# Performance work log

Measured on AMD Instinct MI355X. Metric: run time of the kernel, lower is better.

The kernel has to match this reference:

```python
import jax, jax.numpy as jnp
import numpy as np

B = 1024        # number of dialogs
MX_LEN = 110    # max utterances per dialog (alpha width hardcoded to 110 in source)
G_DIM = 512     # node feature dim
WP, WF = 10, 10 # past / future window
ALPHA_W = 110
NEG = -1e9


def setup_inputs() -> dict:
    key = jax.random.key(0)
    k1, k2, k3 = jax.random.split(key, 3)
    node_features = jax.random.normal(k1, (B, MX_LEN, G_DIM), dtype=jnp.float32)
    var = 2.0 / (G_DIM + G_DIM)  # matches torch init: normal_(0, var)
    weight = jax.random.normal(k2, (G_DIM, G_DIM), dtype=jnp.float32) * var
    text_len = jax.random.randint(k3, (B,), 1, MX_LEN + 1)
    return {"node_features": node_features, "weight": weight, "text_len": text_len}


def reference(node_features, weight, text_len):
    Bsz, L, D = node_features.shape
    # att_matrix[b, l] = weight @ node_features[b, l]
    att = jnp.einsum('de,ble->bld', weight, node_features)            # [B, L, D]
    # score[b, j, l] = att[b, l] . node_features[b, j]
    scores = jnp.einsum('bld,bjd->bjl', att, node_features)           # [B, J, Lkey]
    j = jnp.arange(L)[:, None]   # query position
    l = jnp.arange(L)[None, :]   # key position
    lens = text_len[:, None, None]                                    # [B, 1, 1]
    # window: s = max(0, j-wp), e = min(j+wf, cur_len-1); valid only for j < cur_len
    mask = (l >= j - WP) & (l <= j + WF) & (l <= lens - 1) & (j <= lens - 1)
    probs = jax.nn.softmax(jnp.where(mask, scores, NEG), axis=-1)
    probs = jnp.where(mask, probs, 0.0)                               # [B, L, L]
    # alpha is [mx_len, 110] per batch, zero outside window; stack over batch
    alpha = jnp.zeros((Bsz, L, ALPHA_W), dtype=probs.dtype).at[:, :, :L].set(probs)
    return alpha
```

## Files before the change

### kernel.cpp

```cpp
#include <hip/hip_runtime.h>
#include <stdint.h>

#define L_SZ 110
#define D_SZ 512
#define OUT_W 110
#define A_STRIDE 520
#define C_STRIDE 136
#define A_ROWS 112
#define ATT_ROWS 112
#define NF_ROWS 112
#define G3_ST 40

typedef __attribute__((ext_vector_type(8))) __bf16 bf16x8;
typedef __attribute__((ext_vector_type(4))) __bf16 bf16x4;
typedef __attribute__((ext_vector_type(4))) float f32x4;

__global__ __launch_bounds__(256) void wconv_kernel(const float* __restrict__ W,
                                                    __bf16* __restrict__ wbf) {
    int idx = blockIdx.x * 256 + threadIdx.x;
    float4 w = ((const float4*)W)[idx];
    bf16x4 o;
    o[0] = (__bf16)w.x; o[1] = (__bf16)w.y; o[2] = (__bf16)w.z; o[3] = (__bf16)w.w;
    ((bf16x4*)wbf)[idx] = o;
}

__global__ __launch_bounds__(256, 3) void att_gemm5_kernel(
    const float* __restrict__ nf, const __bf16* __restrict__ wbf,
    const int* __restrict__ tlenp, __bf16* __restrict__ attws,
    __bf16* __restrict__ nfbf)
{
    __shared__ __bf16 A_lds[112 * G3_ST];
    __shared__ __bf16 B_lds[128 * G3_ST];

    const int b   = blockIdx.y;
    const int cg  = blockIdx.x;
    const int tid = threadIdx.x;
    const int lane = tid & 63;
    const int wave = tid >> 6;
    const int l15  = lane & 15;
    const int quad = lane >> 4;

    int len = tlenp[b];
    if (len > L_SZ) len = L_SZ;
    if (len < 1) len = 1;
    const int T = (len + 15) >> 4;
    const int rows_needed = T << 4;

    const float* nfb = nf + (size_t)b * (L_SZ * D_SZ);

    const int r0 = tid >> 2;
    const int c8 = (tid & 3) << 3;
    const int rows2[2] = { r0, r0 + 64 };
    int stat[2];
    #pragma unroll
    for (int s = 0; s < 2; ++s) {
        int r = rows2[s];
        stat[s] = (r >= rows_needed) ? 0 : ((r < L_SZ) ? 1 : 2);
    }

    f32x4 acc[7][2];
    const f32x4 fz = {0.f, 0.f, 0.f, 0.f};
    #pragma unroll
    for (int m = 0; m < 7; ++m) { acc[m][0] = fz; acc[m][1] = fz; }

    float4 abuf[2][2];
    bf16x8 bbuf[2];

    auto load_tiles = [&](int k0) {
        #pragma unroll
        for (int s = 0; s < 2; ++s) {
            if (stat[s] == 1) {
                const float* ap = nfb + (size_t)rows2[s] * D_SZ + k0 + c8;
                abuf[s][0] = *(const float4*)ap;
                abuf[s][1] = *(const float4*)(ap + 4);
            }
            bbuf[s] = *(const bf16x8*)&wbf[(size_t)(cg * 128 + rows2[s]) * D_SZ + k0 + c8];
        }
    };
    auto store_tiles = [&](int kcur) {
        #pragma unroll
        for (int s = 0; s < 2; ++s) {
            if (stat[s]) {
                bf16x8 o;
                if (stat[s] == 1) {
                    o[0]=(__bf16)abuf[s][0].x; o[1]=(__bf16)abuf[s][0].y;
                    o[2]=(__bf16)abuf[s][0].z; o[3]=(__bf16)abuf[s][0].w;
                    o[4]=(__bf16)abuf[s][1].x; o[5]=(__bf16)abuf[s][1].y;
                    o[6]=(__bf16)abuf[s][1].z; o[7]=(__bf16)abuf[s][1].w;
                } else {
                    o[0]=o[1]=o[2]=o[3]=o[4]=o[5]=o[6]=o[7]=(__bf16)0.0f;
                }
                *(bf16x8*)&A_lds[rows2[s] * G3_ST + c8] = o;
                if (cg == 0) {
                    *(bf16x8*)&nfbf[((size_t)b * NF_ROWS + rows2[s]) * D_SZ + kcur + c8] = o;
                }
            }
            *(bf16x8*)&B_lds[rows2[s] * G3_ST + c8] = bbuf[s];
        }
    };

    load_tiles(0);
    for (int kt = 0; kt < 16; ++kt) {
        store_tiles(kt << 5);
        __syncthreads();
        if (kt < 15) load_tiles((kt + 1) << 5);
        bf16x8 bfr[2];
        #pragma unroll
        for (int ni = 0; ni < 2; ++ni)
            bfr[ni] = *(const bf16x8*)&B_lds[(wave * 32 + ni * 16 + l15) * G3_ST + quad * 8];
        #pragma unroll
        for (int m = 0; m < 7; ++m) {
            if (m < T) {
                bf16x8 af = *(const bf16x8*)&A_lds[(m * 16 + l15) * G3_ST + quad * 8];
                acc[m][0] = __builtin_amdgcn_mfma_f32_16x16x32_bf16(af, bfr[0], acc[m][0], 0, 0, 0);
                acc[m][1] = __builtin_amdgcn_mfma_f32_16x16x32_bf16(af, bfr[1], acc[m][1], 0, 0, 0);
            }
        }
        __syncthreads();
    }

    __bf16* tw = &A_lds[wave * 16 * G3_ST];
    const size_t obase = (size_t)b * (ATT_ROWS * D_SZ) + cg * 128 + wave * 32;
    const int erow = lane >> 2;
    const int ec8  = (lane & 3) << 3;
    #pragma unroll
    for (int m = 0; m < 7; ++m) {
        if (m < T) {
            #pragma unroll
            for (int ni = 0; ni < 2; ++ni)
                #pragma unroll
                for (int r = 0; r < 4; ++r)
                    tw[(quad * 4 + r) * G3_ST + ni * 16 + l15] = (__bf16)acc[m][ni][r];
            bf16x8 v = *(const bf16x8*)&tw[erow * G3_ST + ec8];
            *(bf16x8*)&attws[obase + (size_t)(m * 16 + erow) * D_SZ + ec8] = v;
        }
    }
}

__global__ __launch_bounds__(256) void band3_kernel(
    const __bf16* __restrict__ nfbf, const __bf16* __restrict__ attws,
    const int* __restrict__ tlenp, float* __restrict__ out)
{
    const int half = blockIdx.x;
    const int b = blockIdx.y;
    const int tid = threadIdx.x;
    const int lane = tid & 63;
    const int wave = tid >> 6;
    const int l15 = lane & 15;
    const int quad = lane >> 4;

    int len = tlenp[b];
    if (len > L_SZ) len = L_SZ;
    if (len < 1) len = 1;
    const int T = (len + 15) >> 4;

    const int tj = half * 4 + wave;
    if (tj >= T) return;

    float* outb = out + (size_t)b * (L_SZ * OUT_W);

    int jr = (tj << 4) + l15;
    if (jr > L_SZ - 1) jr = L_SZ - 1;
    const __bf16* apt = &nfbf[((size_t)b * NF_ROWS + jr) * D_SZ + (quad << 3)];

    bool tv[3];
    const __bf16* bpt[3];
    #pragma unroll
    for (int t = 0; t < 3; ++t) {
        int tl = tj - 1 + t;
        tv[t] = (tl >= 0) && (tl < T);
        bpt[t] = tv[t] ? &attws[((size_t)b * ATT_ROWS + (tl << 4) + l15) * D_SZ + (quad << 3)]
                       : apt;
    }

    const f32x4 fz = {0.f, 0.f, 0.f, 0.f};
    f32x4 accS[3] = {fz, fz, fz};

    bf16x8 afA, afB, bfA[3], bfB[3];
    afA = *(const bf16x8*)(apt);
    #pragma unroll
    for (int t = 0; t < 3; ++t) if (tv[t]) bfA[t] = *(const bf16x8*)(bpt[t]);

    #pragma unroll
    for (int kt = 0; kt < 16; ++kt) {
        const int knext = (kt + 1) << 5;
        if ((kt & 1) == 0) {
            if (kt < 15) {
                afB = *(const bf16x8*)(apt + knext);
                #pragma unroll
                for (int t = 0; t < 3; ++t) if (tv[t]) bfB[t] = *(const bf16x8*)(bpt[t] + knext);
            }
            #pragma unroll
            for (int t = 0; t < 3; ++t)
                if (tv[t]) accS[t] = __builtin_amdgcn_mfma_f32_16x16x32_bf16(afA, bfA[t], accS[t], 0, 0, 0);
        } else {
            if (kt < 15) {
                afA = *(const bf16x8*)(apt + knext);
                #pragma unroll
                for (int t = 0; t < 3; ++t) if (tv[t]) bfA[t] = *(const bf16x8*)(bpt[t] + knext);
            }
            #pragma unroll
            for (int t = 0; t < 3; ++t)
                if (tv[t]) accS[t] = __builtin_amdgcn_mfma_f32_16x16x32_bf16(afB, bfB[t], accS[t], 0, 0, 0);
        }
    }

    #pragma unroll
    for (int r = 0; r < 4; ++r) {
        int j = tj * 16 + quad * 4 + r;
        float v[3]; bool mk[3];
        float vmax = -3.0e38f;
        #pragma unroll
        for (int t = 0; t < 3; ++t) {
            int tl = tj - 1 + t;
            int l = tl * 16 + l15;
            bool in = tv[t] && (j < len) && (l < len)
                      && (l >= j - 10) && (l <= j + 10);
            float val = in ? accS[t][r] : -3.0e38f;
            mk[t] = in; v[t] = val;
            vmax = fmaxf(vmax, val);
        }
        #pragma unroll
        for (int s = 1; s < 16; s <<= 1)
            vmax = fmaxf(vmax, __shfl_xor(vmax, s, 16));
        float e[3]; float esum = 0.f;
        #pragma unroll
        for (int t = 0; t < 3; ++t) {
            e[t] = mk[t] ? __expf(v[t] - vmax) : 0.f;
            esum += e[t];
        }
        #pragma unroll
        for (int s = 1; s < 16; s <<= 1)
            esum += __shfl_xor(esum, s, 16);
        float inv = (esum > 0.f) ? (1.0f / esum) : 0.f;
        if (j < OUT_W) {
            #pragma unroll
            for (int t = 0; t < 3; ++t) {
                if (tv[t]) {
                    int l = (tj - 1 + t) * 16 + l15;
                    if (l < OUT_W) outb[(size_t)j * OUT_W + l] = e[t] * inv;
                }
            }
        }
    }
}

__global__ __launch_bounds__(256, 3) void att_gemm3_kernel(
    const float* __restrict__ nf, const __bf16* __restrict__ wbf,
    const int* __restrict__ tlenp, __bf16* __restrict__ attws)
{
    __shared__ __bf16 A_lds[112 * G3_ST];
    __shared__ __bf16 B_lds[128 * G3_ST];

    const int b   = blockIdx.y;
    const int cg  = blockIdx.x;
    const int tid = threadIdx.x;
    const int lane = tid & 63;
    const int wave = tid >> 6;
    const int l15  = lane & 15;
    const int quad = lane >> 4;

    int len = tlenp[b];
    if (len > L_SZ) len = L_SZ;
    if (len < 1) len = 1;
    const int T = (len + 15) >> 4;
    const int rows_needed = T << 4;

    const float* nfb = nf + (size_t)b * (L_SZ * D_SZ);

    const int r0 = tid >> 2;
    const int c8 = (tid & 3) << 3;
    const int rows2[2] = { r0, r0 + 64 };
    int stat[2];
    #pragma unroll
    for (int s = 0; s < 2; ++s) {
        int r = rows2[s];
        stat[s] = (r >= rows_needed) ? 0 : ((r < L_SZ) ? 1 : 2);
    }

    f32x4 acc[7][2];
    const f32x4 fz = {0.f, 0.f, 0.f, 0.f};
    #pragma unroll
    for (int m = 0; m < 7; ++m) { acc[m][0] = fz; acc[m][1] = fz; }

    float4 abuf[2][2];
    bf16x8 bbuf[2];

    auto load_tiles = [&](int k0) {
        #pragma unroll
        for (int s = 0; s < 2; ++s) {
            if (stat[s] == 1) {
                const float* ap = nfb + (size_t)rows2[s] * D_SZ + k0 + c8;
                abuf[s][0] = *(const float4*)ap;
                abuf[s][1] = *(const float4*)(ap + 4);
            }
            bbuf[s] = *(const bf16x8*)&wbf[(size_t)(cg * 128 + rows2[s]) * D_SZ + k0 + c8];
        }
    };
    auto store_tiles = [&]() {
        #pragma unroll
        for (int s = 0; s < 2; ++s) {
            if (stat[s]) {
                bf16x8 o;
                if (stat[s] == 1) {
                    o[0]=(__bf16)abuf[s][0].x; o[1]=(__bf16)abuf[s][0].y;
                    o[2]=(__bf16)abuf[s][0].z; o[3]=(__bf16)abuf[s][0].w;
                    o[4]=(__bf16)abuf[s][1].x; o[5]=(__bf16)abuf[s][1].y;
                    o[6]=(__bf16)abuf[s][1].z; o[7]=(__bf16)abuf[s][1].w;
                } else {
                    o[0]=o[1]=o[2]=o[3]=o[4]=o[5]=o[6]=o[7]=(__bf16)0.0f;
                }
                *(bf16x8*)&A_lds[rows2[s] * G3_ST + c8] = o;
            }
            *(bf16x8*)&B_lds[rows2[s] * G3_ST + c8] = bbuf[s];
        }
    };

    load_tiles(0);
    for (int kt = 0; kt < 16; ++kt) {
        store_tiles();
        __syncthreads();
        if (kt < 15) load_tiles((kt + 1) << 5);
        bf16x8 bfr[2];
        #pragma unroll
        for (int ni = 0; ni < 2; ++ni)
            bfr[ni] = *(const bf16x8*)&B_lds[(wave * 32 + ni * 16 + l15) * G3_ST + quad * 8];
        #pragma unroll
        for (int m = 0; m < 7; ++m) {
            if (m < T) {
                bf16x8 af = *(const bf16x8*)&A_lds[(m * 16 + l15) * G3_ST + quad * 8];
                acc[m][0] = __builtin_amdgcn_mfma_f32_16x16x32_bf16(af, bfr[0], acc[m][0], 0, 0, 0);
                acc[m][1] = __builtin_amdgcn_mfma_f32_16x16x32_bf16(af, bfr[1], acc[m][1], 0, 0, 0);
            }
        }
        __syncthreads();
    }

    __bf16* tw = &A_lds[wave * 16 * G3_ST];
    const size_t obase = (size_t)b * (ATT_ROWS * D_SZ) + cg * 128 + wave * 32;
    const int erow = lane >> 2;
    const int ec8  = (lane & 3) << 3;
    #pragma unroll
    for (int m = 0; m < 7; ++m) {
        if (m < T) {
            #pragma unroll
            for (int ni = 0; ni < 2; ++ni)
                #pragma unroll
                for (int r = 0; r < 4; ++r)
                    tw[(quad * 4 + r) * G3_ST + ni * 16 + l15] = (__bf16)acc[m][ni][r];
            bf16x8 v = *(const bf16x8*)&tw[erow * G3_ST + ec8];
            *(bf16x8*)&attws[obase + (size_t)(m * 16 + erow) * D_SZ + ec8] = v;
        }
    }
}

__global__ __launch_bounds__(256) void band_kernel(
    const float* __restrict__ nf, const __bf16* __restrict__ attws,
    const int* __restrict__ tlenp, float* __restrict__ out)
{
    const int b = blockIdx.x;
    const int tid = threadIdx.x;
    const int lane = tid & 63;
    const int wave = tid >> 6;
    const int l15 = lane & 15;
    const int quad = lane >> 4;

    int len = tlenp[b];
    if (len > L_SZ) len = L_SZ;
    if (len < 1) len = 1;
    const int T = (len + 15) >> 4;

    const float* nfb = nf + (size_t)b * (L_SZ * D_SZ);
    float* outb = out + (size_t)b * (L_SZ * OUT_W);

    const f32x4 fz = {0.f, 0.f, 0.f, 0.f};
    f32x4 accS[2][3];
    #pragma unroll
    for (int i = 0; i < 2; ++i)
        #pragma unroll
        for (int t = 0; t < 3; ++t) accS[i][t] = fz;

    #pragma unroll
    for (int i = 0; i < 2; ++i) {
        const int tj = wave + (i << 2);
        if (tj < T) {
            int jr = (tj << 4) + l15;
            if (jr > L_SZ - 1) jr = L_SZ - 1;
            const float* ap0 = &nfb[(size_t)jr * D_SZ];
            for (int k0 = 0; k0 < D_SZ; k0 += 32) {
                float4 a0 = *(const float4*)(ap0 + k0 + (quad << 3));
                float4 a1 = *(const float4*)(ap0 + k0 + (quad << 3) + 4);
                bf16x8 af;
                af[0] = (__bf16)a0.x; af[1] = (__bf16)a0.y;
                af[2] = (__bf16)a0.z; af[3] = (__bf16)a0.w;
                af[4] = (__bf16)a1.x; af[5] = (__bf16)a1.y;
                af[6] = (__bf16)a1.z; af[7] = (__bf16)a1.w;
                #pragma unroll
                for (int t = 0; t < 3; ++t) {
                    int tl = tj - 1 + t;
                    if (tl >= 0 && tl < T) {
                        bf16x8 bfr = *(const bf16x8*)&attws[((size_t)b * ATT_ROWS + (tl << 4) + l15) * D_SZ + k0 + (quad << 3)];
                        accS[i][t] = __builtin_amdgcn_mfma_f32_16x16x32_bf16(
                            af, bfr, accS[i][t], 0, 0, 0);
                    }
                }
            }
        }
    }

    #pragma unroll
    for (int i = 0; i < 2; ++i) {
        int tj = wave + 4 * i;
        if (tj >= T) continue;
        #pragma unroll
        for (int r = 0; r < 4; ++r) {
            int j = tj * 16 + quad * 4 + r;
            float v[3]; bool mk[3];
            float vmax = -3.0e38f;
            #pragma unroll
            for (int t = 0; t < 3; ++t) {
                int tl = tj - 1 + t;
                int l = tl * 16 + l15;
                bool in = (tl >= 0) && (tl < T) && (j < len) && (l < len)
                          && (l >= j - 10) && (l <= j + 10);
                float val = in ? accS[i][t][r] : -3.0e38f;
                mk[t] = in; v[t] = val;
                vmax = fmaxf(vmax, val);
            }
            #pragma unroll
            for (int s = 1; s < 16; s <<= 1)
                vmax = fmaxf(vmax, __shfl_xor(vmax, s, 16));
            float e[3]; float esum = 0.f;
            #pragma unroll
            for (int t = 0; t < 3; ++t) {
                e[t] = mk[t] ? __expf(v[t] - vmax) : 0.f;
                esum += e[t];
            }
            #pragma unroll
            for (int s = 1; s < 16; s <<= 1)
                esum += __shfl_xor(esum, s, 16);
            float inv = (esum > 0.f) ? (1.0f / esum) : 0.f;
            if (j < OUT_W) {
                #pragma unroll
                for (int t = 0; t < 3; ++t) {
                    int tl = tj - 1 + t;
                    if (tl >= 0 && tl < T) {
                        int l = tl * 16 + l15;
                        if (l < OUT_W) outb[(size_t)j * OUT_W + l] = e[t] * inv;
                    }
                }
            }
        }
    }
}

__global__ __launch_bounds__(256, 1) void edgeatt_kernel(
    const float* __restrict__ nf, const float* __restrict__ Wf,
    const __bf16* __restrict__ wbf, const int* __restrict__ tlenp,
    float* __restrict__ out, int use_wb)
{
    __shared__ __bf16 A_lds[A_ROWS * A_STRIDE];
    __shared__ __bf16 C_lds[A_ROWS * C_STRIDE];

    const int b = blockIdx.x;
    const int tid = threadIdx.x;
    const int lane = tid & 63;
    const int wave = tid >> 6;
    const int l15 = lane & 15;
    const int quad = lane >> 4;

    int len = tlenp[b];
    if (len > L_SZ) len = L_SZ;
    if (len < 1) len = 1;
    const int T = (len + 15) >> 4;

    const float* nfb = nf + (size_t)b * (L_SZ * D_SZ);
    float* outb = out + (size_t)b * (L_SZ * OUT_W);

    {
        int total4 = len * (D_SZ / 4);
        for (int idx = tid; idx < total4; idx += 256) {
            int row = idx >> 7;
            int c4 = idx & 127;
            float4 v = ((const float4*)nfb)[row * 128 + c4];
            bf16x4 o;
            o[0]=(__bf16)v.x; o[1]=(__bf16)v.y; o[2]=(__bf16)v.z; o[3]=(__bf16)v.w;
            *(bf16x4*)&A_lds[row * A_STRIDE + c4 * 4] = o;
        }
        int zr = 16 * T - len;
        if (zr > 0) {
            int per = A_STRIDE / 4;
            int totalz = zr * per;
            for (int idx = tid; idx < totalz; idx += 256) {
                int row = len + idx / per;
                int c4 = idx % per;
                bf16x4 z; z[0]=z[1]=z[2]=z[3]=(__bf16)0.0f;
                *(bf16x4*)&A_lds[row * A_STRIDE + c4 * 4] = z;
            }
        }
    }
    __syncthreads();

    const int wm = wave >> 1, wn = wave & 1;
    const int h = (T + 1) >> 1;
    const int mt_lo = (wm == 0) ? 0 : h;
    const int nmt = ((wm == 0) ? h : T) - mt_lo;

    const f32x4 fzero = {0.f, 0.f, 0.f, 0.f};
    f32x4 accS[2][3];
    #pragma unroll
    for (int i = 0; i < 2; ++i)
        #pragma unroll
        for (int t = 0; t < 3; ++t) accS[i][t] = fzero;

    for (int c = 0; c < 4; ++c) {
        const int d0 = c * 128;
        f32x4 acc1[4][4];
        #pragma unroll
        for (int mi = 0; mi < 4; ++mi)
            #pragma unroll
            for (int ni = 0; ni < 4; ++ni) acc1[mi][ni] = fzero;

        if (nmt > 0) {
            for (int k0 = 0; k0 < D_SZ; k0 += 32) {
                bf16x8 afrag[4], bfrag[4];
                #pragma unroll
                for (int ni = 0; ni < 4; ++ni) {
                    int d = d0 + (wn * 4 + ni) * 16 + l15;
                    if (use_wb) {
                        bfrag[ni] = *(const bf16x8*)&wbf[(size_t)d * D_SZ + k0 + quad * 8];
                    } else {
                        const float* wp = &Wf[(size_t)d * D_SZ + k0 + quad * 8];
                        float4 w0 = *(const float4*)wp;
                        float4 w1 = *(const float4*)(wp + 4);
                        bf16x8 bb;
                        bb[0]=(__bf16)w0.x; bb[1]=(__bf16)w0.y; bb[2]=(__bf16)w0.z; bb[3]=(__bf16)w0.w;
                        bb[4]=(__bf16)w1.x; bb[5]=(__bf16)w1.y; bb[6]=(__bf16)w1.z; bb[7]=(__bf16)w1.w;
                        bfrag[ni] = bb;
                    }
                }
                #pragma unroll
                for (int mi = 0; mi < 4; ++mi) {
                    if (mi < nmt) {
                        int row = (mt_lo + mi) * 16 + l15;
                        afrag[mi] = *(const bf16x8*)&A_lds[row * A_STRIDE + k0 + quad * 8];
                    }
                }
                #pragma unroll
                for (int mi = 0; mi < 4; ++mi) {
                    if (mi < nmt) {
                        #pragma unroll
                        for (int ni = 0; ni < 4; ++ni)
                            acc1[mi][ni] = __builtin_amdgcn_mfma_f32_16x16x32_bf16(
                                afrag[mi], bfrag[ni], acc1[mi][ni], 0, 0, 0);
                    }
                }
            }
        }
        __syncthreads();

        #pragma unroll
        for (int mi = 0; mi < 4; ++mi) {
            if (mi < nmt) {
                int lbase = (mt_lo + mi) * 16 + quad * 4;
                #pragma unroll
                for (int ni = 0; ni < 4; ++ni) {
                    int dloc = (wn * 4 + ni) * 16 + l15;
                    #pragma unroll
                    for (int r = 0; r < 4; ++r)
                        C_lds[(lbase + r) * C_STRIDE + dloc] = (__bf16)acc1[mi][ni][r];
                }
            }
        }
        __syncthreads();

        for (int kk = 0; kk < 128; kk += 32) {
            #pragma unroll
            for (int i = 0; i < 2; ++i) {
                int tj = wave + 4 * i;
                if (tj < T) {
                    bf16x8 aj = *(const bf16x8*)&A_lds[(tj * 16 + l15) * A_STRIDE + d0 + kk + quad * 8];
                    #pragma unroll
                    for (int t = 0; t < 3; ++t) {
                        int tl = tj - 1 + t;
                        if (tl >= 0 && tl < T) {
                            bf16x8 bj = *(const bf16x8*)&C_lds[(tl * 16 + l15) * C_STRIDE + kk + quad * 8];
                            accS[i][t] = __builtin_amdgcn_mfma_f32_16x16x32_bf16(
                                aj, bj, accS[i][t], 0, 0, 0);
                        }
                    }
                }
            }
        }
        __syncthreads();
    }

    #pragma unroll
    for (int i = 0; i < 2; ++i) {
        int tj = wave + 4 * i;
        if (tj >= T) continue;
        #pragma unroll
        for (int r = 0; r < 4; ++r) {
            int j = tj * 16 + quad * 4 + r;
            float v[3]; bool mk[3];
            float vmax = -3.0e38f;
            #pragma unroll
            for (int t = 0; t < 3; ++t) {
                int tl = tj - 1 + t;
                int l = tl * 16 + l15;
                bool in = (tl >= 0) && (tl < T) && (j < len) && (l < len)
                          && (l >= j - 10) && (l <= j + 10);
                float val = in ? accS[i][t][r] : -3.0e38f;
                mk[t] = in; v[t] = val;
                vmax = fmaxf(vmax, val);
            }
            #pragma unroll
            for (int s = 1; s < 16; s <<= 1)
                vmax = fmaxf(vmax, __shfl_xor(vmax, s, 16));
            float e[3]; float esum = 0.f;
            #pragma unroll
            for (int t = 0; t < 3; ++t) {
                e[t] = mk[t] ? __expf(v[t] - vmax) : 0.f;
                esum += e[t];
            }
            #pragma unroll
            for (int s = 1; s < 16; s <<= 1)
                esum += __shfl_xor(esum, s, 16);
            float inv = (esum > 0.f) ? (1.0f / esum) : 0.f;
            if (j < OUT_W) {
                #pragma unroll
                for (int t = 0; t < 3; ++t) {
                    int tl = tj - 1 + t;
                    if (tl >= 0 && tl < T) {
                        int l = tl * 16 + l15;
                        if (l < OUT_W) outb[(size_t)j * OUT_W + l] = e[t] * inv;
                    }
                }
            }
        }
    }
}

extern "C" void kernel_launch(void* const* d_in, const int* in_sizes, int n_in,
                              void* d_out, int out_size, void* d_ws, size_t ws_size,
                              hipStream_t stream) {
    const float* nf = (const float*)d_in[0];
    const float* W  = (const float*)d_in[1];
    const int* tl   = (const int*)d_in[2];
    float* out      = (float*)d_out;
    __bf16* wbf     = (__bf16*)d_ws;
    const int B = in_sizes[2];

    const size_t wb_bytes  = (size_t)D_SZ * D_SZ * sizeof(__bf16);
    const size_t att_bytes = (size_t)B * ATT_ROWS * D_SZ * sizeof(__bf16);
    const size_t nf_bytes  = (size_t)B * NF_ROWS * D_SZ * sizeof(__bf16);
    const int use_wb = (ws_size >= wb_bytes) ? 1 : 0;
    const int fast   = (use_wb && ws_size >= wb_bytes + att_bytes) ? 1 : 0;
    const int fast2  = (fast && ws_size >= wb_bytes + att_bytes + nf_bytes) ? 1 : 0;

    hipMemsetAsync(d_out, 0, (size_t)out_size * sizeof(float), stream);

    if (use_wb) {
        hipLaunchKernelGGL(wconv_kernel, dim3(256), dim3(256), 0, stream, W, wbf);
    }
    if (fast2) {
        __bf16* attws = (__bf16*)((char*)d_ws + wb_bytes);
        __bf16* nfbf  = (__bf16*)((char*)d_ws + wb_bytes + att_bytes);
        hipLaunchKernelGGL(att_gemm5_kernel, dim3(4, B), dim3(256), 0, stream, nf, wbf, tl, attws, nfbf);
        hipLaunchKernelGGL(band3_kernel, dim3(2, B), dim3(256), 0, stream, nfbf, attws, tl, out);
    } else if (fast) {
        __bf16* attws = (__bf16*)((char*)d_ws + wb_bytes);
        hipLaunchKernelGGL(att_gemm3_kernel, dim3(4, B), dim3(256), 0, stream, nf, wbf, tl, attws);
        hipLaunchKernelGGL(band_kernel, dim3(B), dim3(256), 0, stream, nf, attws, tl, out);
    } else {
        hipLaunchKernelGGL(edgeatt_kernel, dim3(B), dim3(256), 0, stream,
                           nf, W, wbf, tl, out, use_wb);
    }
}
```

Measured before the change: 470.0 us.

## Split att GEMM rows across blocks and stage band tiles in LDS

The attention GEMM now splits each dialog's rows into two 64-row halves, giving 8 blocks per dialog. Halves with no valid rows exit early, and the smaller accumulator and LDS footprint permit a higher occupancy hint. The band kernel is restructured to one block per 16-row query tile: waves cooperatively stage the query tile and three key tiles into swizzled LDS, compute scores with MFMA, and then do the masked softmax across all 256 threads. This aims to improve parallelism and load efficiency, at the cost of re-reading the W tiles in both GEMM halves and using 64KB of LDS per band block.

```diff
diff --git a/kernel.cpp b/kernel.cpp
--- a/kernel.cpp
+++ b/kernel.cpp
@@ -24,16 +24,17 @@
     ((bf16x4*)wbf)[idx] = o;
 }
 
-__global__ __launch_bounds__(256, 3) void att_gemm5_kernel(
+__global__ __launch_bounds__(256, 5) void att_gemm6_kernel(
     const float* __restrict__ nf, const __bf16* __restrict__ wbf,
     const int* __restrict__ tlenp, __bf16* __restrict__ attws,
     __bf16* __restrict__ nfbf)
 {
-    __shared__ __bf16 A_lds[112 * G3_ST];
+    __shared__ __bf16 A_lds[64 * G3_ST];
     __shared__ __bf16 B_lds[128 * G3_ST];
 
     const int b   = blockIdx.y;
-    const int cg  = blockIdx.x;
+    const int cg  = blockIdx.x & 3;
+    const int mh  = blockIdx.x >> 2;
     const int tid = threadIdx.x;
     const int lane = tid & 63;
     const int wave = tid >> 6;
@@ -44,59 +45,55 @@
     if (len > L_SZ) len = L_SZ;
     if (len < 1) len = 1;
     const int T = (len + 15) >> 4;
+    if (T <= mh * 4) return;
+    const int Tl = (T - mh * 4 < 4) ? (T - mh * 4) : 4;
     const int rows_needed = T << 4;
+    const int rbase = mh << 6;
 
     const float* nfb = nf + (size_t)b * (L_SZ * D_SZ);
 
     const int r0 = tid >> 2;
     const int c8 = (tid & 3) << 3;
-    const int rows2[2] = { r0, r0 + 64 };
-    int stat[2];
-    #pragma unroll
-    for (int s = 0; s < 2; ++s) {
-        int r = rows2[s];
-        stat[s] = (r >= rows_needed) ? 0 : ((r < L_SZ) ? 1 : 2);
-    }
-
-    f32x4 acc[7][2];
+    const int ga = rbase + r0;
+    const int astat = (ga >= rows_needed) ? 0 : ((ga < L_SZ) ? 1 : 2);
+
+    f32x4 acc[4][2];
     const f32x4 fz = {0.f, 0.f, 0.f, 0.f};
     #pragma unroll
-    for (int m = 0; m < 7; ++m) { acc[m][0] = fz; acc[m][1] = fz; }
-
-    float4 abuf[2][2];
+    for (int m = 0; m < 4; ++m) { acc[m][0] = fz; acc[m][1] = fz; }
+
+    float4 abuf[2];
     bf16x8 bbuf[2];
 
     auto load_tiles = [&](int k0) {
-        #pragma unroll
-        for (int s = 0; s < 2; ++s) {
-            if (stat[s] == 1) {
-                const float* ap = nfb + (size_t)rows2[s] * D_SZ + k0 + c8;
-                abuf[s][0] = *(const float4*)ap;
-                abuf[s][1] = *(const float4*)(ap + 4);
-            }
-            bbuf[s] = *(const bf16x8*)&wbf[(size_t)(cg * 128 + rows2[s]) * D_SZ + k0 + c8];
-        }
+        if (astat == 1) {
+            const float* ap = nfb + (size_t)ga * D_SZ + k0 + c8;
+            abuf[0] = *(const float4*)ap;
+            abuf[1] = *(const float4*)(ap + 4);
+        }
+        #pragma unroll
+        for (int s = 0; s < 2; ++s)
+            bbuf[s] = *(const bf16x8*)&wbf[(size_t)(cg * 128 + r0 + 64 * s) * D_SZ + k0 + c8];
     };
     auto store_tiles = [&](int kcur) {
-        #pragma unroll
-        for (int s = 0; s < 2; ++s) {
-            if (stat[s]) {
-                bf16x8 o;
-                if (stat[s] == 1) {
-                    o[0]=(__bf16)abuf[s][0].x; o[1]=(__bf16)abuf[s][0].y;
-                    o[2]=(__bf16)abuf[s][0].z; o[3]=(__bf16)abuf[s][0].w;
-                    o[4]=(__bf16)abuf[s][1].x; o[5]=(__bf16)abuf[s][1].y;
-                    o[6]=(__bf16)abuf[s][1].z; o[7]=(__bf16)abuf[s][1].w;
-                } else {
-                    o[0]=o[1]=o[2]=o[3]=o[4]=o[5]=o[6]=o[7]=(__bf16)0.0f;
-                }
-                *(bf16x8*)&A_lds[rows2[s] * G3_ST + c8] = o;
-                if (cg == 0) {
-                    *(bf16x8*)&nfbf[((size_t)b * NF_ROWS + rows2[s]) * D_SZ + kcur + c8] = o;
-                }
-            }
-            *(bf16x8*)&B_lds[rows2[s] * G3_ST + c8] = bbuf[s];
-        }
+        if (astat) {
+            bf16x8 o;
+            if (astat == 1) {
+                o[0]=(__bf16)abuf[0].x; o[1]=(__bf16)abuf[0].y;
+                o[2]=(__bf16)abuf[0].z; o[3]=(__bf16)abuf[0].w;
+                o[4]=(__bf16)abuf[1].x; o[5]=(__bf16)abuf[1].y;
+                o[6]=(__bf16)abuf[1].z; o[7]=(__bf16)abuf[1].w;
+            } else {
+                o[0]=o[1]=o[2]=o[3]=o[4]=o[5]=o[6]=o[7]=(__bf16)0.0f;
+            }
+            *(bf16x8*)&A_lds[r0 * G3_ST + c8] = o;
+            if (cg == 0) {
+                *(bf16x8*)&nfbf[((size_t)b * NF_ROWS + ga) * D_SZ + kcur + c8] = o;
+            }
+        }
+        #pragma unroll
+        for (int s = 0; s < 2; ++s)
+            *(bf16x8*)&B_lds[(r0 + 64 * s) * G3_ST + c8] = bbuf[s];
     };
 
     load_tiles(0);
@@ -109,8 +106,8 @@
         for (int ni = 0; ni < 2; ++ni)
             bfr[ni] = *(const bf16x8*)&B_lds[(wave * 32 + ni * 16 + l15) * G3_ST + quad * 8];
         #pragma unroll
-        for (int m = 0; m < 7; ++m) {
-            if (m < T) {
+        for (int m = 0; m < 4; ++m) {
+            if (m < Tl) {
                 bf16x8 af = *(const bf16x8*)&A_lds[(m * 16 + l15) * G3_ST + quad * 8];
                 acc[m][0] = __builtin_amdgcn_mfma_f32_16x16x32_bf16(af, bfr[0], acc[m][0], 0, 0, 0);
                 acc[m][1] = __builtin_amdgcn_mfma_f32_16x16x32_bf16(af, bfr[1], acc[m][1], 0, 0, 0);
@@ -124,25 +121,28 @@
     const int erow = lane >> 2;
     const int ec8  = (lane & 3) << 3;
     #pragma unroll
-    for (int m = 0; m < 7; ++m) {
-        if (m < T) {
+    for (int m = 0; m < 4; ++m) {
+        if (m < Tl) {
             #pragma unroll
             for (int ni = 0; ni < 2; ++ni)
                 #pragma unroll
                 for (int r = 0; r < 4; ++r)
                     tw[(quad * 4 + r) * G3_ST + ni * 16 + l15] = (__bf16)acc[m][ni][r];
             bf16x8 v = *(const bf16x8*)&tw[erow * G3_ST + ec8];
-            *(bf16x8*)&attws[obase + (size_t)(m * 16 + erow) * D_SZ + ec8] = v;
+            *(bf16x8*)&attws[obase + (size_t)(rbase + m * 16 + erow) * D_SZ + ec8] = v;
         }
     }
 }
 
-__global__ __launch_bounds__(256) void band3_kernel(
+__global__ __launch_bounds__(256) void band4_kernel(
     const __bf16* __restrict__ nfbf, const __bf16* __restrict__ attws,
     const int* __restrict__ tlenp, float* __restrict__ out)
 {
-    const int half = blockIdx.x;
-    const int b = blockIdx.y;
+    __shared__ __bf16 KV[64 * D_SZ];
+    __shared__ float S[16 * 52];
+
+    const int tj = blockIdx.x;
+    const int b  = blockIdx.y;
     const int tid = threadIdx.x;
     const int lane = tid & 63;
     const int wave = tid >> 6;
@@ -153,93 +153,90 @@
     if (len > L_SZ) len = L_SZ;
     if (len < 1) len = 1;
     const int T = (len + 15) >> 4;
-
-    const int tj = half * 4 + wave;
     if (tj >= T) return;
 
-    float* outb = out + (size_t)b * (L_SZ * OUT_W);
-
-    int jr = (tj << 4) + l15;
-    if (jr > L_SZ - 1) jr = L_SZ - 1;
-    const __bf16* apt = &nfbf[((size_t)b * NF_ROWS + jr) * D_SZ + (quad << 3)];
-
     bool tv[3];
-    const __bf16* bpt[3];
     #pragma unroll
     for (int t = 0; t < 3; ++t) {
         int tl = tj - 1 + t;
         tv[t] = (tl >= 0) && (tl < T);
-        bpt[t] = tv[t] ? &attws[((size_t)b * ATT_ROWS + (tl << 4) + l15) * D_SZ + (quad << 3)]
-                       : apt;
-    }
-
-    const f32x4 fz = {0.f, 0.f, 0.f, 0.f};
-    f32x4 accS[3] = {fz, fz, fz};
-
-    bf16x8 afA, afB, bfA[3], bfB[3];
-    afA = *(const bf16x8*)(apt);
-    #pragma unroll
-    for (int t = 0; t < 3; ++t) if (tv[t]) bfA[t] = *(const bf16x8*)(bpt[t]);
-
-    #pragma unroll
-    for (int kt = 0; kt < 16; ++kt) {
-        const int knext = (kt + 1) << 5;
-        if ((kt & 1) == 0) {
-            if (kt < 15) {
-                afB = *(const bf16x8*)(apt + knext);
-                #pragma unroll
-                for (int t = 0; t < 3; ++t) if (tv[t]) bfB[t] = *(const bf16x8*)(bpt[t] + knext);
-            }
-            #pragma unroll
-            for (int t = 0; t < 3; ++t)
-                if (tv[t]) accS[t] = __builtin_amdgcn_mfma_f32_16x16x32_bf16(afA, bfA[t], accS[t], 0, 0, 0);
-        } else {
-            if (kt < 15) {
-                afA = *(const bf16x8*)(apt + knext);
-                #pragma unroll
-                for (int t = 0; t < 3; ++t) if (tv[t]) bfA[t] = *(const bf16x8*)(bpt[t] + knext);
-            }
-            #pragma unroll
-            for (int t = 0; t < 3; ++t)
-                if (tv[t]) accS[t] = __builtin_amdgcn_mfma_f32_16x16x32_bf16(afB, bfB[t], accS[t], 0, 0, 0);
-        }
-    }
-
-    #pragma unroll
-    for (int r = 0; r < 4; ++r) {
-        int j = tj * 16 + quad * 4 + r;
-        float v[3]; bool mk[3];
-        float vmax = -3.0e38f;
+    }
+
+    {
+        const int bt = wave - 1;
+        const bool do_stage = (wave == 0) || tv[bt];
+        if (do_stage) {
+            const __bf16* gsrc = (wave == 0)
+                ? &nfbf[((size_t)b * NF_ROWS + (tj << 4)) * D_SZ]
+                : &attws[((size_t)b * ATT_ROWS + ((tj - 1 + bt) << 4)) * D_SZ];
+            __bf16* lbase = &KV[(size_t)(wave * 16) * D_SZ];
+            bf16x8 st[16];
+            #pragma unroll
+            for (int i = 0; i < 16; ++i)
+                st[i] = *(const bf16x8*)&gsrc[(size_t)i * D_SZ + (lane << 3)];
+            #pragma unroll
+            for (int i = 0; i < 16; ++i) {
+                int ch = lane ^ (i & 7);
+                *(bf16x8*)&lbase[i * D_SZ + (ch << 3)] = st[i];
+            }
+        }
+    }
+    __syncthreads();
+
+    if (wave < 3 && tv[wave]) {
+        const __bf16* arow = &KV[0];
+        const __bf16* brow = &KV[(size_t)((wave + 1) * 16) * D_SZ];
+        const f32x4 fz = {0.f, 0.f, 0.f, 0.f};
+        f32x4 acc = fz;
+        #pragma unroll
+        for (int kt = 0; kt < 16; ++kt) {
+            int ca = (kt * 4 + quad) ^ (l15 & 7);
+            bf16x8 af = *(const bf16x8*)&arow[l15 * D_SZ + (ca << 3)];
+            bf16x8 bf = *(const bf16x8*)&brow[l15 * D_SZ + (ca << 3)];
+            acc = __builtin_amdgcn_mfma_f32_16x16x32_bf16(af, bf, acc, 0, 0, 0);
+        }
+        #pragma unroll
+        for (int r = 0; r < 4; ++r)
+            S[(quad * 4 + r) * 52 + wave * 16 + l15] = acc[r];
+    }
+    __syncthreads();
+
+    const int srow = tid >> 4;
+    const int sc   = tid & 15;
+    const int j = (tj << 4) + srow;
+    float* outb = out + (size_t)b * (L_SZ * OUT_W);
+
+    float v[3]; bool mk[3];
+    float vmax = -3.0e38f;
+    #pragma unroll
+    for (int t = 0; t < 3; ++t) {
+        int tl = tj - 1 + t;
+        int l = (tl << 4) + sc;
+        bool in = tv[t] && (j < len) && (l < len)
+                  && (l >= j - 10) && (l <= j + 10);
+        float val = in ? S[srow * 52 + t * 16 + sc] : -3.0e38f;
+        mk[t] = in; v[t] = val;
+        vmax = fmaxf(vmax, val);
+    }
+    #pragma unroll
+    for (int s = 1; s < 16; s <<= 1)
+        vmax = fmaxf(vmax, __shfl_xor(vmax, s, 16));
+    float e[3]; float esum = 0.f;
+    #pragma unroll
+    for (int t = 0; t < 3; ++t) {
+        e[t] = mk[t] ? __expf(v[t] - vmax) : 0.f;
+        esum += e[t];
+    }
+    #pragma unroll
+    for (int s = 1; s < 16; s <<= 1)
+        esum += __shfl_xor(esum, s, 16);
+    float inv = (esum > 0.f) ? (1.0f / esum) : 0.f;
+    if (j < OUT_W) {
         #pragma unroll
         for (int t = 0; t < 3; ++t) {
-            int tl = tj - 1 + t;
-            int l = tl * 16 + l15;
-            bool in = tv[t] && (j < len) && (l < len)
-                      && (l >= j - 10) && (l <= j + 10);
-            float val = in ? accS[t][r] : -3.0e38f;
-            mk[t] = in; v[t] = val;
-            vmax = fmaxf(vmax, val);
-        }
-        #pragma unroll
-        for (int s = 1; s < 16; s <<= 1)
-            vmax = fmaxf(vmax, __shfl_xor(vmax, s, 16));
-        float e[3]; float esum = 0.f;
-        #pragma unroll
-        for (int t = 0; t < 3; ++t) {
-            e[t] = mk[t] ? __expf(v[t] - vmax) : 0.f;
-            esum += e[t];
-        }
-        #pragma unroll
-        for (int s = 1; s < 16; s <<= 1)
-            esum += __shfl_xor(esum, s, 16);
-        float inv = (esum > 0.f) ? (1.0f / esum) : 0.f;
-        if (j < OUT_W) {
-            #pragma unroll
-            for (int t = 0; t < 3; ++t) {
-                if (tv[t]) {
-                    int l = (tj - 1 + t) * 16 + l15;
-                    if (l < OUT_W) outb[(size_t)j * OUT_W + l] = e[t] * inv;
-                }
+            if (tv[t]) {
+                int l = ((tj - 1 + t) << 4) + sc;
+                if (l < OUT_W) outb[(size_t)j * OUT_W + l] = e[t] * inv;
             }
         }
     }
@@ -666,8 +663,8 @@
     if (fast2) {
         __bf16* attws = (__bf16*)((char*)d_ws + wb_bytes);
         __bf16* nfbf  = (__bf16*)((char*)d_ws + wb_bytes + att_bytes);
-        hipLaunchKernelGGL(att_gemm5_kernel, dim3(4, B), dim3(256), 0, stream, nf, wbf, tl, attws, nfbf);
-        hipLaunchKernelGGL(band3_kernel, dim3(2, B), dim3(256), 0, stream, nfbf, attws, tl, out);
+        hipLaunchKernelGGL(att_gemm6_kernel, dim3(8, B), dim3(256), 0, stream, nf, wbf, tl, attws, nfbf);
+        hipLaunchKernelGGL(band4_kernel, dim3(7, B), dim3(256), 0, stream, nfbf, attws, tl, out);
     } else if (fast) {
         __bf16* attws = (__bf16*)((char*)d_ws + wb_bytes);
         hipLaunchKernelGGL(att_gemm3_kernel, dim3(4, B), dim3(256), 0, stream, nf, wbf, tl, attws);
```

After: 494.9 us. 1.05x slower.
